# Performance work log

Measured on AMD Instinct MI355X. Metric: run time of the kernel, lower is better.

Reference implementation:

```python
import jax, jax.numpy as jnp
import numpy as np

DIM = 768
NUM_HEADS = 12
LATENT_LEN = 32


def setup_inputs() -> dict:
    key = jax.random.key(0)
    k1, k2, k3, k4 = jax.random.split(key, 4)
    x = jax.random.normal(k1, (32, 4096, DIM), dtype=jnp.float32)
    latent = jax.random.normal(k2, (1, LATENT_LEN, DIM), dtype=jnp.float32) * 0.02
    # torch nn.Linear(dim, dim): weight [out, in], bias [out]
    bound = 1.0 / np.sqrt(DIM)
    v_w = jax.random.uniform(k3, (DIM, DIM), dtype=jnp.float32, minval=-bound, maxval=bound)
    v_b = jax.random.uniform(k4, (DIM,), dtype=jnp.float32, minval=-bound, maxval=bound)
    return {"x": x, "latent": latent, "v_w": v_w, "v_b": v_b}


def reference(x, latent, v_w, v_b):
    B, N, C = x.shape
    H = NUM_HEADS
    hd = C // H
    L = LATENT_LEN
    chunk = C // L
    scale = hd ** (-0.5)

    # q: [L, H, hd] from latent (shared across batch)
    q = latent[0].reshape(L, H, hd)
    # k: [B, N, H, hd]
    k = x.reshape(B, N, H, hd)
    # attn logits: [B, H, L, N]
    attn = jnp.einsum("lhd,bnhd->bhln", q * scale, k)
    attn = jax.nn.softmax(attn, axis=-1)
    attn = attn.mean(axis=1)  # [B, L, N] (head-mean before value matmul)

    # v: Linear then split channels by latent_len -> [B, L, N, chunk]
    v = (jnp.einsum("bnc,dc->bnd", x, v_w) + v_b).reshape(B, N, L, chunk)
    out = jnp.einsum("bln,blnc->blc", attn, v.transpose(0, 2, 1, 3))
    return out.reshape(B, 1, C)
```

## Files before the change

### kernel.cpp

```cpp
#include <hip/hip_runtime.h>
#include <cstdint>


typedef short bf16x8 __attribute__((ext_vector_type(8)));
typedef float f32x4 __attribute__((ext_vector_type(4)));

#define MFMA16(a, b, c) __builtin_amdgcn_mfma_f32_16x16x32_bf16((a), (b), (c), 0, 0, 0)

__device__ __forceinline__ uint32_t pk_bf16(float a, float b) {
    return __builtin_amdgcn_perm(__float_as_uint(b), __float_as_uint(a), 0x07060302u);
}
__device__ __forceinline__ unsigned short bf16_trunc(float f) {
    return (unsigned short)(__float_as_uint(f) >> 16);
}
__device__ __forceinline__ float bf16_lo(uint32_t u) { return __uint_as_float(u << 16); }
__device__ __forceinline__ float bf16_hi(uint32_t u) { return __uint_as_float(u & 0xffff0000u); }

__global__ __launch_bounds__(256)
void k0_init(const float* __restrict__ latent, unsigned short* __restrict__ qbf,
             float* __restrict__ sums)
{
    int i = blockIdx.x * 256 + threadIdx.x;
    if (i < 12288) sums[i] = 0.f;
    int l = i / 768;
    int r = i - l * 768;
    int h = r >> 6, d = r & 63;
    qbf[(h * 32 + l) * 64 + d] = bf16_trunc(latent[i] * 0.125f);
}

__global__ __launch_bounds__(256)
void k1_logits(const float* __restrict__ x, const unsigned short* __restrict__ qbf,
               unsigned short* __restrict__ E, unsigned short* __restrict__ xT,
               float* __restrict__ sums)
{
    const int bx  = blockIdx.x;
    const int b   = bx >> 7;
    const int r7  = bx & 127;
    const int n0  = (r7 >> 1 >> 0) << 6;
    (void)n0;
    const int b2   = bx / 192;
    const int rem  = bx - b2 * 192;
    const int nt   = rem >> 2;
    (void)b2; (void)nt;
    const int ntile = bx & 63;
    const int bh    = bx >> 6;
    const int hb    = bh % 3;
    const int bb    = bh / 3;
    const int nn0   = ntile << 6;

    const int tid  = threadIdx.x;
    const int wv   = tid >> 6;
    const int lane = tid & 63;
    const int quad = lane >> 4;
    const int lc   = lane & 15;

    __shared__ __align__(16) unsigned short x_lds[4][64][72];
    __shared__ float bsum[4][32][4];

    for (int i = tid; i < 4096; i += 256) {
        const int nn = i >> 6;
        const int j  = i & 63;
        const int h  = j >> 4, f4 = j & 15;
        float4 xv = *(const float4*)&x[(size_t)(bb * 4096 + nn0 + nn) * 768 + hb * 256 + j * 4];
        uint2 p;
        p.x = pk_bf16(xv.x, xv.y);
        p.y = pk_bf16(xv.z, xv.w);
        *(uint2*)&x_lds[h][nn][f4 * 4] = p;
    }
    __syncthreads();

    const int n  = nn0 + wv * 16 + lc;
    const int td = lane;

    #pragma unroll
    for (int h = 0; h < 4; ++h) {
        const int hg = hb * 4 + h;
        const unsigned short* qh = qbf + hg * 2048;
        bf16x8 a00 = *(const bf16x8*)&qh[lc * 64 + quad * 8];
        bf16x8 a01 = *(const bf16x8*)&qh[lc * 64 + 32 + quad * 8];
        bf16x8 a10 = *(const bf16x8*)&qh[(16 + lc) * 64 + quad * 8];
        bf16x8 a11 = *(const bf16x8*)&qh[(16 + lc) * 64 + 32 + quad * 8];
        bf16x8 b0  = *(const bf16x8*)&x_lds[h][wv * 16 + lc][quad * 8];
        bf16x8 b1  = *(const bf16x8*)&x_lds[h][wv * 16 + lc][32 + quad * 8];

        f32x4 c0 = {0.f, 0.f, 0.f, 0.f};
        f32x4 c1 = {0.f, 0.f, 0.f, 0.f};
        c0 = MFMA16(a00, b0, c0);
        c0 = MFMA16(a01, b1, c0);
        c1 = MFMA16(a10, b0, c1);
        c1 = MFMA16(a11, b1, c1);

        unsigned short* Eh = E + (size_t)((bb * 12 + hg) * 32) * 4096;
        float sv[8];
        #pragma unroll
        for (int r = 0; r < 4; ++r) {
            uint32_t u0 = __float_as_uint(__expf(c0[r]));
            uint32_t u1 = __float_as_uint(__expf(c1[r]));
            Eh[(quad * 4 + r) * 4096 + n]      = (unsigned short)(u0 >> 16);
            Eh[(16 + quad * 4 + r) * 4096 + n] = (unsigned short)(u1 >> 16);
            sv[r]     = __uint_as_float(u0 & 0xffff0000u);
            sv[4 + r] = __uint_as_float(u1 & 0xffff0000u);
        }
        #pragma unroll
        for (int m = 1; m < 16; m <<= 1) {
            #pragma unroll
            for (int k = 0; k < 8; ++k) sv[k] += __shfl_xor(sv[k], m);
        }
        if (lc == 0) {
            #pragma unroll
            for (int r = 0; r < 4; ++r) {
                bsum[h][quad * 4 + r][wv]      = sv[r];
                bsum[h][16 + quad * 4 + r][wv] = sv[4 + r];
            }
        }

        unsigned short* xTrow = xT + ((size_t)bb * 768 + hg * 64 + td) * 4096 + nn0;
        #pragma unroll
        for (int half = 0; half < 2; ++half) {
            const int nc = wv + half * 4;
            unsigned short r0 = x_lds[h][nc * 8 + 0][td], r1 = x_lds[h][nc * 8 + 1][td];
            unsigned short r2 = x_lds[h][nc * 8 + 2][td], r3 = x_lds[h][nc * 8 + 3][td];
            unsigned short r4 = x_lds[h][nc * 8 + 4][td], r5 = x_lds[h][nc * 8 + 5][td];
            unsigned short r6 = x_lds[h][nc * 8 + 6][td], r7 = x_lds[h][nc * 8 + 7][td];
            uint4 w;
            w.x = (uint32_t)r0 | ((uint32_t)r1 << 16);
            w.y = (uint32_t)r2 | ((uint32_t)r3 << 16);
            w.z = (uint32_t)r4 | ((uint32_t)r5 << 16);
            w.w = (uint32_t)r6 | ((uint32_t)r7 << 16);
            *(uint4*)&xTrow[nc * 8] = w;
        }
    }

    __syncthreads();
    if (tid < 128) {
        const int h = tid >> 5, l = tid & 31;
        atomicAdd(&sums[(bb * 12 + hb * 4 + h) * 32 + l],
                  bsum[h][l][0] + bsum[h][l][1] + bsum[h][l][2] + bsum[h][l][3]);
    }
}

__global__ __launch_bounds__(256)
void kw_weights(const unsigned short* __restrict__ E, const float* __restrict__ sums,
                unsigned short* __restrict__ W)
{
    const int b = blockIdx.x >> 5;
    const int l = blockIdx.x & 31;
    const int tid = threadIdx.x;

    const unsigned short* Eb = E + (size_t)(b * 384 + l) * 4096;
    __shared__ float rsl[12];
    if (tid < 12) rsl[tid] = 1.0f / (12.0f * sums[(b * 12 + tid) * 32 + l]);
    __syncthreads();

    float acc[16];
    #pragma unroll
    for (int i = 0; i < 16; ++i) acc[i] = 0.f;
    #pragma unroll
    for (int h = 0; h < 12; ++h) {
        float r = rsl[h];
        const uint4* p = (const uint4*)(Eb + (size_t)h * 131072 + tid * 16);
        uint4 u0 = p[0], u1 = p[1];
        acc[0] += bf16_lo(u0.x) * r;  acc[1] += bf16_hi(u0.x) * r;
        acc[2] += bf16_lo(u0.y) * r;  acc[3] += bf16_hi(u0.y) * r;
        acc[4] += bf16_lo(u0.z) * r;  acc[5] += bf16_hi(u0.z) * r;
        acc[6] += bf16_lo(u0.w) * r;  acc[7] += bf16_hi(u0.w) * r;
        acc[8] += bf16_lo(u1.x) * r;  acc[9] += bf16_hi(u1.x) * r;
        acc[10] += bf16_lo(u1.y) * r; acc[11] += bf16_hi(u1.y) * r;
        acc[12] += bf16_lo(u1.z) * r; acc[13] += bf16_hi(u1.z) * r;
        acc[14] += bf16_lo(u1.w) * r; acc[15] += bf16_hi(u1.w) * r;
    }
    uint4 o0, o1;
    o0.x = pk_bf16(acc[0], acc[1]);   o0.y = pk_bf16(acc[2], acc[3]);
    o0.z = pk_bf16(acc[4], acc[5]);   o0.w = pk_bf16(acc[6], acc[7]);
    o1.x = pk_bf16(acc[8], acc[9]);   o1.y = pk_bf16(acc[10], acc[11]);
    o1.z = pk_bf16(acc[12], acc[13]); o1.w = pk_bf16(acc[14], acc[15]);
    uint4* wp = (uint4*)(W + (size_t)(b * 32 + l) * 4096 + tid * 16);
    wp[0] = o0; wp[1] = o1;
}

__global__ __launch_bounds__(64)
void yacc_kernel(const unsigned short* __restrict__ xT, const unsigned short* __restrict__ W,
                 float* __restrict__ yws)
{
    const int bx  = blockIdx.x;
    const int b   = bx / 96;
    const int rem = bx - b * 96;
    const int ct  = rem % 12;
    const int g   = rem / 12;
    const int lane = threadIdx.x;
    const int quad = lane >> 4;
    const int lc   = lane & 15;
    const int c0   = ct * 64;
    const int nb   = g * 512;

    const unsigned short* xTb = xT + (size_t)b * 768 * 4096;
    const unsigned short* Wb  = W + (size_t)b * 32 * 4096;

    f32x4 acc[2][4];
    #pragma unroll
    for (int t = 0; t < 2; ++t)
        #pragma unroll
        for (int s = 0; s < 4; ++s) acc[t][s] = (f32x4){0.f, 0.f, 0.f, 0.f};

    for (int kk = 0; kk < 512; kk += 32) {
        const int n = nb + kk + quad * 8;
        bf16x8 a0 = *(const bf16x8*)&Wb[lc * 4096 + n];
        bf16x8 a1 = *(const bf16x8*)&Wb[(16 + lc) * 4096 + n];
        #pragma unroll
        for (int s = 0; s < 4; ++s) {
            bf16x8 bb = *(const bf16x8*)&xTb[(size_t)(c0 + s * 16 + lc) * 4096 + n];
            acc[0][s] = MFMA16(a0, bb, acc[0][s]);
            acc[1][s] = MFMA16(a1, bb, acc[1][s]);
        }
    }

    float* yp = yws + (size_t)((g * 32 + b) * 32) * 768;
    #pragma unroll
    for (int t = 0; t < 2; ++t)
        #pragma unroll
        for (int s = 0; s < 4; ++s)
            #pragma unroll
            for (int r = 0; r < 4; ++r)
                yp[(t * 16 + quad * 4 + r) * 768 + c0 + s * 16 + lc] = acc[t][s][r];
}

__global__ __launch_bounds__(256)
void out_kernel(const float* __restrict__ yws, const float* __restrict__ vw,
                const float* __restrict__ vb, float* __restrict__ out)
{
    const int b = blockIdx.x >> 5;
    const int l = blockIdx.x & 31;
    const int tid = threadIdx.x;
    __shared__ float y_lds[768];
    for (int c = tid; c < 768; c += 256) {
        float v = 0.f;
        #pragma unroll
        for (int g = 0; g < 8; ++g)
            v += yws[(size_t)((g * 32 + b) * 32 + l) * 768 + c];
        y_lds[c] = v;
    }
    __syncthreads();
    const int wv = tid >> 6, lane = tid & 63;
    for (int i = wv; i < 24; i += 4) {
        const int row = l * 24 + i;
        const float* wr = vw + row * 768;
        float p = 0.f;
        #pragma unroll
        for (int j = 0; j < 12; ++j)
            p += y_lds[j * 64 + lane] * wr[j * 64 + lane];
        #pragma unroll
        for (int m = 1; m < 64; m <<= 1) p += __shfl_xor(p, m);
        if (lane == 0) out[b * 768 + row] = p + vb[row];
    }
}

extern "C" void kernel_launch(void* const* d_in, const int* in_sizes, int n_in,
                              void* d_out, int out_size, void* d_ws, size_t ws_size,
                              hipStream_t stream)
{
    const float* x      = (const float*)d_in[0];
    const float* latent = (const float*)d_in[1];
    const float* vw     = (const float*)d_in[2];
    const float* vb     = (const float*)d_in[3];
    float* out = (float*)d_out;

    char* ws = (char*)d_ws;
    unsigned short* E    = (unsigned short*)ws;
    unsigned short* W    = (unsigned short*)(ws + 100663296);
    float*          yws  = (float*)(ws + 109051904);
    unsigned short* xT   = (unsigned short*)(ws + 134217728);
    unsigned short* qbf  = (unsigned short*)(ws + 335544320);
    float*          sums = (float*)(ws + 335609856);

    k0_init<<<dim3(96), dim3(256), 0, stream>>>(latent, qbf, sums);
    k1_logits<<<dim3(6144), dim3(256), 0, stream>>>(x, qbf, E, xT, sums);
    kw_weights<<<dim3(1024), dim3(256), 0, stream>>>(E, sums, W);
    yacc_kernel<<<dim3(3072), dim3(64), 0, stream>>>(xT, W, yws);
    out_kernel<<<dim3(1024), dim3(256), 0, stream>>>(yws, vw, vb, out);
}
```

Baseline: 763.7 us.

## Store bf16 x in natural layout and transpose in LDS inside yacc

The logits kernel now writes a plain bf16 copy of x in its original row-major layout, replacing the strided transposed store it did before. The accumulation kernel becomes a 256-thread tiled GEMM that stages W and x tiles in shared memory. It assembles the transposed MFMA B operands from LDS with scalar 16-bit reads. The aim is to turn the uncoalesced transpose writes into coalesced global traffic, at the cost of extra LDS work and bank conflicts in yacc.

Result: faster. 738.0 us (-3.4%).

```diff
diff --git a/kernel.cpp b/kernel.cpp
--- a/kernel.cpp
+++ b/kernel.cpp
@@ -30,18 +30,10 @@
 
 __global__ __launch_bounds__(256)
 void k1_logits(const float* __restrict__ x, const unsigned short* __restrict__ qbf,
-               unsigned short* __restrict__ E, unsigned short* __restrict__ xT,
+               unsigned short* __restrict__ E, unsigned short* __restrict__ xbf,
                float* __restrict__ sums)
 {
-    const int bx  = blockIdx.x;
-    const int b   = bx >> 7;
-    const int r7  = bx & 127;
-    const int n0  = (r7 >> 1 >> 0) << 6;
-    (void)n0;
-    const int b2   = bx / 192;
-    const int rem  = bx - b2 * 192;
-    const int nt   = rem >> 2;
-    (void)b2; (void)nt;
+    const int bx    = blockIdx.x;
     const int ntile = bx & 63;
     const int bh    = bx >> 6;
     const int hb    = bh % 3;
@@ -61,16 +53,17 @@
         const int nn = i >> 6;
         const int j  = i & 63;
         const int h  = j >> 4, f4 = j & 15;
-        float4 xv = *(const float4*)&x[(size_t)(bb * 4096 + nn0 + nn) * 768 + hb * 256 + j * 4];
+        const size_t gof = (size_t)(bb * 4096 + nn0 + nn) * 768 + hb * 256 + j * 4;
+        float4 xv = *(const float4*)&x[gof];
         uint2 p;
         p.x = pk_bf16(xv.x, xv.y);
         p.y = pk_bf16(xv.z, xv.w);
         *(uint2*)&x_lds[h][nn][f4 * 4] = p;
-    }
-    __syncthreads();
-
-    const int n  = nn0 + wv * 16 + lc;
-    const int td = lane;
+        *(uint2*)&xbf[gof] = p;
+    }
+    __syncthreads();
+
+    const int n = nn0 + wv * 16 + lc;
 
     #pragma unroll
     for (int h = 0; h < 4; ++h) {
@@ -112,22 +105,6 @@
                 bsum[h][quad * 4 + r][wv]      = sv[r];
                 bsum[h][16 + quad * 4 + r][wv] = sv[4 + r];
             }
-        }
-
-        unsigned short* xTrow = xT + ((size_t)bb * 768 + hg * 64 + td) * 4096 + nn0;
-        #pragma unroll
-        for (int half = 0; half < 2; ++half) {
-            const int nc = wv + half * 4;
-            unsigned short r0 = x_lds[h][nc * 8 + 0][td], r1 = x_lds[h][nc * 8 + 1][td];
-            unsigned short r2 = x_lds[h][nc * 8 + 2][td], r3 = x_lds[h][nc * 8 + 3][td];
-            unsigned short r4 = x_lds[h][nc * 8 + 4][td], r5 = x_lds[h][nc * 8 + 5][td];
-            unsigned short r6 = x_lds[h][nc * 8 + 6][td], r7 = x_lds[h][nc * 8 + 7][td];
-            uint4 w;
-            w.x = (uint32_t)r0 | ((uint32_t)r1 << 16);
-            w.y = (uint32_t)r2 | ((uint32_t)r3 << 16);
-            w.z = (uint32_t)r4 | ((uint32_t)r5 << 16);
-            w.w = (uint32_t)r6 | ((uint32_t)r7 << 16);
-            *(uint4*)&xTrow[nc * 8] = w;
         }
     }
 
@@ -178,50 +155,87 @@
     wp[0] = o0; wp[1] = o1;
 }
 
-__global__ __launch_bounds__(64)
-void yacc_kernel(const unsigned short* __restrict__ xT, const unsigned short* __restrict__ W,
+__global__ __launch_bounds__(256)
+void yacc_kernel(const unsigned short* __restrict__ xbf, const unsigned short* __restrict__ W,
                  float* __restrict__ yws)
 {
-    const int bx  = blockIdx.x;
-    const int b   = bx / 96;
-    const int rem = bx - b * 96;
-    const int ct  = rem % 12;
-    const int g   = rem / 12;
-    const int lane = threadIdx.x;
+    const int bx = blockIdx.x;
+    const int kg = bx & 7;
+    const int bc = bx >> 3;
+    const int cn = bc % 6;
+    const int b  = bc / 6;
+    const int c0 = cn * 128;
+    const int n00 = kg * 512;
+
+    const int tid  = threadIdx.x;
+    const int wv   = tid >> 6;
+    const int lane = tid & 63;
     const int quad = lane >> 4;
     const int lc   = lane & 15;
-    const int c0   = ct * 64;
-    const int nb   = g * 512;
-
-    const unsigned short* xTb = xT + (size_t)b * 768 * 4096;
-    const unsigned short* Wb  = W + (size_t)b * 32 * 4096;
-
-    f32x4 acc[2][4];
+
+    __shared__ __align__(16) unsigned short wl[32][72];
+    __shared__ __align__(16) unsigned short xl[64][130];
+
+    const unsigned short* Wb = W + (size_t)b * 32 * 4096;
+    const unsigned short* xb = xbf + (size_t)b * 4096 * 768;
+
+    f32x4 acc[2][2];
     #pragma unroll
     for (int t = 0; t < 2; ++t)
         #pragma unroll
-        for (int s = 0; s < 4; ++s) acc[t][s] = (f32x4){0.f, 0.f, 0.f, 0.f};
-
-    for (int kk = 0; kk < 512; kk += 32) {
-        const int n = nb + kk + quad * 8;
-        bf16x8 a0 = *(const bf16x8*)&Wb[lc * 4096 + n];
-        bf16x8 a1 = *(const bf16x8*)&Wb[(16 + lc) * 4096 + n];
-        #pragma unroll
-        for (int s = 0; s < 4; ++s) {
-            bf16x8 bb = *(const bf16x8*)&xTb[(size_t)(c0 + s * 16 + lc) * 4096 + n];
-            acc[0][s] = MFMA16(a0, bb, acc[0][s]);
-            acc[1][s] = MFMA16(a1, bb, acc[1][s]);
-        }
-    }
-
-    float* yp = yws + (size_t)((g * 32 + b) * 32) * 768;
+        for (int cs = 0; cs < 2; ++cs) acc[t][cs] = (f32x4){0.f, 0.f, 0.f, 0.f};
+
+    const int wrow = tid >> 3, wchk = tid & 7;
+
+    for (int it = 0; it < 8; ++it) {
+        const int n0 = n00 + it * 64;
+        uint4 wreg = *(const uint4*)&Wb[(size_t)wrow * 4096 + n0 + wchk * 8];
+        uint4 xreg[4];
+        #pragma unroll
+        for (int k = 0; k < 4; ++k) {
+            const int m = tid + k * 256;
+            xreg[k] = *(const uint4*)&xb[(size_t)(n0 + (m >> 4)) * 768 + c0 + (m & 15) * 8];
+        }
+        __syncthreads();
+        *(uint4*)&wl[wrow][wchk * 8] = wreg;
+        #pragma unroll
+        for (int k = 0; k < 4; ++k) {
+            const int m = tid + k * 256;
+            *(uint4*)&xl[m >> 4][(m & 15) * 8] = xreg[k];
+        }
+        __syncthreads();
+
+        #pragma unroll
+        for (int ks = 0; ks < 2; ++ks) {
+            bf16x8 a0 = *(const bf16x8*)&wl[lc][ks * 32 + quad * 8];
+            bf16x8 a1 = *(const bf16x8*)&wl[16 + lc][ks * 32 + quad * 8];
+            #pragma unroll
+            for (int cs = 0; cs < 2; ++cs) {
+                const int cc = wv * 32 + cs * 16 + lc;
+                const unsigned short* col = &xl[ks * 32 + quad * 8][cc];
+                uint32_t e0 = col[0],       e1 = col[130];
+                uint32_t e2 = col[2 * 130], e3 = col[3 * 130];
+                uint32_t e4 = col[4 * 130], e5 = col[5 * 130];
+                uint32_t e6 = col[6 * 130], e7 = col[7 * 130];
+                union { uint32_t u[4]; bf16x8 v; } bbu;
+                bbu.u[0] = e0 | (e1 << 16);
+                bbu.u[1] = e2 | (e3 << 16);
+                bbu.u[2] = e4 | (e5 << 16);
+                bbu.u[3] = e6 | (e7 << 16);
+                acc[0][cs] = MFMA16(a0, bbu.v, acc[0][cs]);
+                acc[1][cs] = MFMA16(a1, bbu.v, acc[1][cs]);
+            }
+        }
+    }
+
+    float* yp = yws + (size_t)((kg * 32 + b) * 32) * 768;
     #pragma unroll
     for (int t = 0; t < 2; ++t)
         #pragma unroll
-        for (int s = 0; s < 4; ++s)
+        for (int cs = 0; cs < 2; ++cs)
             #pragma unroll
             for (int r = 0; r < 4; ++r)
-                yp[(t * 16 + quad * 4 + r) * 768 + c0 + s * 16 + lc] = acc[t][s][r];
+                yp[(t * 16 + quad * 4 + r) * 768 + c0 + wv * 32 + cs * 16 + lc] = acc[t][cs][r];
 }
 
 __global__ __launch_bounds__(256)
@@ -268,13 +282,13 @@
     unsigned short* E    = (unsigned short*)ws;
     unsigned short* W    = (unsigned short*)(ws + 100663296);
     float*          yws  = (float*)(ws + 109051904);
-    unsigned short* xT   = (unsigned short*)(ws + 134217728);
+    unsigned short* xbf  = (unsigned short*)(ws + 134217728);
     unsigned short* qbf  = (unsigned short*)(ws + 335544320);
     float*          sums = (float*)(ws + 335609856);
 
     k0_init<<<dim3(96), dim3(256), 0, stream>>>(latent, qbf, sums);
-    k1_logits<<<dim3(6144), dim3(256), 0, stream>>>(x, qbf, E, xT, sums);
+    k1_logits<<<dim3(6144), dim3(256), 0, stream>>>(x, qbf, E, xbf, sums);
     kw_weights<<<dim3(1024), dim3(256), 0, stream>>>(E, sums, W);
-    yacc_kernel<<<dim3(3072), dim3(64), 0, stream>>>(xT, W, yws);
+    yacc_kernel<<<dim3(1536), dim3(256), 0, stream>>>(xbf, W, yws);
     out_kernel<<<dim3(1024), dim3(256), 0, stream>>>(yws, vw, vb, out);
 }
```
